# Performance work log

Measured on AMD Instinct MI355X. Metric: run time of the kernel, lower is better.

The kernel has to match this reference:

```python
import jax, jax.numpy as jnp
import numpy as np

MAX_N = 21
COORD = 3
TOTAL_T = 100
K_RANK = 3
POWER_STEPS = 10


def _recon_single(D, Wt, u_noise, x_noise):
    """D, Wt: [N,N]; u_noise: [K_RANK,N]; x_noise: [N,3]. Returns X: [N,3]."""
    N = MAX_N
    # dist_to_gram (classical MDS double-centering)
    D_row = jnp.sum(D, 0, keepdims=True) / N
    D_col = jnp.sum(D, 1, keepdims=True) / N
    D_mean = jnp.sum(D) / (N * N)
    B = -0.5 * (D - D_row - D_col + D_mean)
    # low_rank_approx_power: k=3 deflated power iterations, 10 steps each
    A = B
    us = []
    for i in range(K_RANK):
        u = u_noise[i]
        for _ in range(POWER_STEPS):
            # F.normalize(u, dim=0, p=2, eps=0.001)
            u = u / jnp.maximum(jnp.linalg.norm(u), 1e-3)
            u = A @ u
        eig_sq = jnp.sum(u * u)
        u = u / jnp.power(eig_sq + 0.01, 0.25)
        us.append(u)
        A = A - jnp.outer(u, u)
    X0 = jnp.stack(us, -1) + x_noise  # [N,3]

    T = jnp.float32(TOTAL_T)

    def energy(X):
        diff = X[None, :, :] - X[:, None, :]          # [N,N,3], D_X[i,j]=||X_j-X_i||^2
        D_X = jnp.sum(diff * diff, -1) + 0.01
        return jnp.sum(Wt * jnp.square(D - D_X))

    def step(X, t):
        g = jax.grad(energy)(X)
        dX = -0.1 * g
        speed = jnp.sqrt(jnp.sum(dX * dX, 1, keepdims=True) + 1e-3)
        alpha_t = 0.1 + (5.0 - 0.1) * ((T - t) / T)
        scale = alpha_t * jnp.tanh(speed / alpha_t) / speed
        return X + dX * scale, None

    X, _ = jax.lax.scan(step, X0, jnp.arange(TOTAL_T, dtype=jnp.float32))
    return X


def _forward(gnn_edge_out, W1, b1, W2, b2, u_noise, x_noise, batch_size):
    h_nf = W1.shape[1]
    # edge_mlp1 (MLP with 1 layer -> Linear + ReLU)
    edge_out = jax.nn.relu(gnn_edge_out @ W1 + b1)                     # [B*N*N, h]
    emb = jnp.sum(edge_out.reshape(batch_size, MAX_N, MAX_N, h_nf), axis=(1, 2))  # [B, h]
    # edge_mlp2 -> symmetrize -> softplus
    e2 = (edge_out @ W2 + b2).reshape(batch_size, MAX_N, MAX_N, 2)
    e2 = e2 + jnp.transpose(e2, (0, 2, 1, 3))
    dw = jax.nn.softplus(e2)
    D_init = dw[..., 0] * (1.0 - jnp.eye(MAX_N, dtype=dw.dtype))       # [B,N,N]
    W = dw[..., 1]                                                     # [B,N,N]
    X_pred = jax.vmap(_recon_single)(D_init, W, u_noise, x_noise)      # [B,N,3]
    return D_init, W, emb, X_pred


def setup_inputs() -> dict:
    key = jax.random.key(0)
    ks = jax.random.split(key, 5)
    B, h_nf = 1024, 256
    n_edges = B * MAX_N * MAX_N
    return {
        "gnn_edge_out": jax.random.normal(ks[0], (n_edges, h_nf), jnp.float32),
        "W1": jax.random.normal(ks[1], (h_nf, h_nf), jnp.float32) * (1.0 / np.sqrt(h_nf)),
        "b1": jnp.zeros((h_nf,), jnp.float32),
        "W2": jax.random.normal(ks[2], (h_nf, 2), jnp.float32) * (1.0 / np.sqrt(h_nf)),
        "b2": jnp.zeros((2,), jnp.float32),
        "u_noise": jax.random.normal(ks[3], (B, K_RANK, MAX_N), jnp.float32),
        "x_noise": jax.random.normal(ks[4], (B, MAX_N, COORD), jnp.float32),
        "batch_size": B,
    }


def reference(gnn_edge_out, W1, b1, W2, b2, u_noise, x_noise, batch_size):
    return _forward(gnn_edge_out, W1, b1, W2, b2, u_noise, x_noise, batch_size)
```

## Files before the change

### kernel.cpp

```cpp
#include <hip/hip_runtime.h>
#include <hip/hip_bf16.h>
#include <math.h>

#define B_SZ 1024
#define NMAX 21
#define NN 441
#define HNF 256
#define TOT_ROWS (B_SZ * NN)
#define TILES_PB 14
#define TROWS 32

typedef short short8 __attribute__((ext_vector_type(8)));
typedef float float4v __attribute__((ext_vector_type(4)));

__device__ __forceinline__ unsigned short f2bf(float x) {
    union { float f; unsigned int u; } v; v.f = x;
    unsigned int r = v.u + 0x7FFFu + ((v.u >> 16) & 1u);
    return (unsigned short)(r >> 16);
}

__device__ __forceinline__ unsigned pk_bf16(float lo, float hi) {
    __hip_bfloat162 h = __float22bfloat162_rn(float2{lo, hi});
    return *reinterpret_cast<unsigned*>(&h);
}

__device__ __forceinline__ float softplus_fast(float x) {
    float e = __builtin_amdgcn_exp2f(-fabsf(x) * 1.44269504088896f);
    float lg = __builtin_amdgcn_logf(1.f + e);
    return fmaxf(x, 0.f) + 0.69314718055995f * lg;
}

__device__ __forceinline__ float tanh_fast(float x) {
    float e = __builtin_amdgcn_exp2f(x * 2.8853900817779268f);
    float q = __builtin_amdgcn_rcpf(e + 1.f);
    return fmaf(-2.f, q, 1.f);
}

__global__ __launch_bounds__(256) void pack_w1(const float* __restrict__ W1,
                                               short* __restrict__ B0p,
                                               float* __restrict__ emb)
{
    int id = blockIdx.x * 256 + threadIdx.x;
    int j = id & 7, l = (id >> 3) & 63, f = (id >> 9) & 15, s = id >> 13;
    int k = s * 32 + ((l >> 4) << 3) + j;
    int c = (f << 4) + (l & 15);
    B0p[id] = (short)f2bf(W1[k * HNF + c]);
    #pragma unroll
    for (int e = 0; e < 4; e++)
        emb[(size_t)e * 65536 + id] = 0.f;
}

__global__ __launch_bounds__(256, 5) void fused_mlp_bf16(
    const float* __restrict__ gnn, const short* __restrict__ B0p,
    const float* __restrict__ b1, const float* __restrict__ W2,
    const float* __restrict__ b2,
    float* __restrict__ Dreg, float* __restrict__ Wreg, float* __restrict__ emb)
{
    __shared__ __align__(16) char ldsbuf[32768];
    float* stage = (float*)ldsbuf;
    short* Abf   = (short*)ldsbuf;
    float (*red0)[32] = (float(*)[32])(ldsbuf + 16384);
    float (*red1)[32] = (float(*)[32])(ldsbuf + 16384 + 512);

    const int t = threadIdx.x;
    const int w = t >> 6, l = t & 63;
    const int batch = blockIdx.x / TILES_PB;
    const int tile  = blockIdx.x % TILES_PB;
    const long row0 = (long)batch * NN + (long)tile * TROWS;
    const int vr = (tile == TILES_PB - 1) ? (NN - (TILES_PB - 1) * TROWS) : TROWS;

    #pragma unroll
    for (int i = 0; i < 8; i++) {
        int r = (w << 3) + i;
        long ar = row0 + r;
        if (ar >= (long)TOT_ROWS) ar = TOT_ROWS - 1;
        const float* gsrc = gnn + ar * HNF + (l << 2);
        __builtin_amdgcn_global_load_lds(
            (const __attribute__((address_space(1))) unsigned*)gsrc,
            (__attribute__((address_space(3))) unsigned*)(stage + (r << 8)),
            16, 0, 0);
    }

    uint2 pv[8];
    asm volatile("s_waitcnt vmcnt(4)" ::: "memory");
    #pragma unroll
    for (int i = 0; i < 4; i++) {
        float4 f = *(const float4*)(stage + (((w << 3) + i) << 8) + (l << 2));
        pv[i].x = pk_bf16(f.x, f.y);
        pv[i].y = pk_bf16(f.z, f.w);
    }
    asm volatile("s_waitcnt vmcnt(0)" ::: "memory");
    #pragma unroll
    for (int i = 4; i < 8; i++) {
        float4 f = *(const float4*)(stage + (((w << 3) + i) << 8) + (l << 2));
        pv[i].x = pk_bf16(f.x, f.y);
        pv[i].y = pk_bf16(f.z, f.w);
    }
    __syncthreads();

    const int kk_s = l >> 3;
    const int fk_s = (l >> 1) & 3;
    const int jh_s = l & 1;
    #pragma unroll
    for (int i = 0; i < 8; i++) {
        int r = (w << 3) + i;
        int di = (((kk_s << 1) + (r >> 4)) << 6) | (fk_s << 4) | (r & 15);
        *(uint2*)((char*)Abf + (((size_t)(di ^ kk_s)) << 4) + (jh_s << 3)) = pv[i];
    }
    __syncthreads();

    const int frow = l & 15;
    const int fk   = l >> 4;

    float4v acc[2][4];
    #pragma unroll
    for (int m = 0; m < 2; m++)
        #pragma unroll
        for (int n = 0; n < 4; n++)
            acc[m][n] = (float4v){0.f, 0.f, 0.f, 0.f};

    #pragma unroll 2
    for (int kk = 0; kk < 8; ++kk) {
        short8 bf[4], af[2];
        #pragma unroll
        for (int n = 0; n < 4; n++) {
            int nf = (w << 2) + n;
            size_t off = (size_t)((((kk << 4) + nf) << 6) | l) << 3;
            bf[n] = *(const short8*)(B0p + off);
        }
        #pragma unroll
        for (int m = 0; m < 2; m++) {
            int di = ((((kk << 1) + m) << 6) | l) ^ kk;
            af[m] = *(const short8*)(Abf + (size_t)di * 8);
        }
        #pragma unroll
        for (int m = 0; m < 2; m++)
            #pragma unroll
            for (int n = 0; n < 4; n++)
                acc[m][n] = __builtin_amdgcn_mfma_f32_16x16x32_bf16(af[m], bf[n], acc[m][n], 0, 0, 0);
    }

    float w20[4], w21[4], b1v[4];
    #pragma unroll
    for (int n = 0; n < 4; n++) {
        int cc = (((w << 2) + n) << 4) + frow;
        b1v[n] = b1[cc];
        w20[n] = W2[2 * cc];
        w21[n] = W2[2 * cc + 1];
    }
    float ps0[2][4], ps1[2][4], embp[4] = {0.f, 0.f, 0.f, 0.f};
    #pragma unroll
    for (int m = 0; m < 2; m++)
        #pragma unroll
        for (int j = 0; j < 4; j++) { ps0[m][j] = 0.f; ps1[m][j] = 0.f; }

    #pragma unroll
    for (int m = 0; m < 2; m++)
        #pragma unroll
        for (int n = 0; n < 4; n++)
            #pragma unroll
            for (int j = 0; j < 4; j++) {
                float h = fmaxf(acc[m][n][j] + b1v[n], 0.f);
                ps0[m][j] += h * w20[n];
                ps1[m][j] += h * w21[n];
                int row = (m << 4) + (fk << 2) + j;
                if (row < vr) embp[n] += h;
            }

    #pragma unroll
    for (int off = 1; off < 16; off <<= 1)
        #pragma unroll
        for (int m = 0; m < 2; m++)
            #pragma unroll
            for (int j = 0; j < 4; j++) {
                ps0[m][j] += __shfl_xor(ps0[m][j], off);
                ps1[m][j] += __shfl_xor(ps1[m][j], off);
            }
    if (frow == 0) {
        #pragma unroll
        for (int m = 0; m < 2; m++)
            #pragma unroll
            for (int j = 0; j < 4; j++) {
                int row = (m << 4) + (fk << 2) + j;
                red0[w][row] = ps0[m][j];
                red1[w][row] = ps1[m][j];
            }
    }

    #pragma unroll
    for (int n = 0; n < 4; n++) {
        embp[n] += __shfl_xor(embp[n], 16);
        embp[n] += __shfl_xor(embp[n], 32);
    }
    if (l < 16) {
        #pragma unroll
        for (int n = 0; n < 4; n++)
            atomicAdd(emb + (size_t)batch * 256 + (((w << 2) + n) << 4) + l, embp[n]);
    }

    __syncthreads();
    if (t < vr) {
        float v0 = b2[0] + red0[0][t] + red0[1][t] + red0[2][t] + red0[3][t];
        float v1 = b2[1] + red1[0][t] + red1[1][t] + red1[2][t] + red1[3][t];
        Dreg[row0 + t] = v0;
        Wreg[row0 + t] = v1;
    }
}

__global__ __launch_bounds__(64) void symrecon_kernel(
    float* __restrict__ Dreg, float* __restrict__ Wreg,
    const float* __restrict__ un, const float* __restrict__ xn,
    float* __restrict__ Xo)
{
    const int b = blockIdx.x, l = threadIdx.x;
    __shared__ float R0[NN], R1[NN];
    __shared__ float Rs[22], Us[22], Xs[3][22];

    float* Db = Dreg + (size_t)b * NN;
    float* Wb = Wreg + (size_t)b * NN;
    for (int idx = l; idx < NN; idx += 64) { R0[idx] = Db[idx]; R1[idx] = Wb[idx]; }
    if (l == 0) { Rs[21] = 0.f; Us[21] = 0.f; Xs[0][21] = 0.f; Xs[1][21] = 0.f; Xs[2][21] = 0.f; }
    __syncthreads();

    const int half = l >> 5;
    const int li   = l & 31;
    const bool act = li < NMAX;
    const int li0  = act ? li : 0;
    const int q0   = half * 11;

    float Drow[11], Wrow[11], WD[11];
    float rsh = 0.f;
    #pragma unroll
    for (int j = 0; j < 11; j++) {
        int q = q0 + j;
        bool v = act && (q < NMAX);
        int qc = v ? q : 0;
        float rd = R0[li0 * NMAX + qc] + R0[qc * NMAX + li0];
        float rw = R1[li0 * NMAX + qc] + R1[qc * NMAX + li0];
        float d  = (v && q != li) ? softplus_fast(rd) : 0.f;
        float wv = v ? softplus_fast(rw) : 0.f;
        Drow[j] = d; Wrow[j] = wv; WD[j] = wv * d;
        rsh += d;
    }
    if (act) {
        #pragma unroll
        for (int j = 0; j < 11; j++) {
            int q = q0 + j;
            if (q < NMAX) {
                Db[li * NMAX + q] = Drow[j];
                Wb[li * NMAX + q] = Wrow[j];
            }
        }
    }

    float rsf = rsh + __shfl_xor(rsh, 32);
    float tot = rsh;
    #pragma unroll
    for (int m = 1; m < 64; m <<= 1) tot += __shfl_xor(tot, m);
    const float mean = tot * (1.f / (float)NN);
    const float rsn  = rsf * (1.f / (float)NMAX);
    if (act && half == 0) Rs[li] = rsn;
    float Arow[11];
    #pragma unroll
    for (int j = 0; j < 11; j++) {
        int q = q0 + j;
        bool v = act && (q < NMAX);
        float rsq = Rs[q];
        Arow[j] = v ? -0.5f * (Drow[j] - rsn - rsq + mean) : 0.f;
    }

    float xc[3];
    #pragma unroll
    for (int e = 0; e < 3; e++) {
        float u = act ? un[(size_t)b * 63 + e * NMAX + li] : 0.f;
        for (int s = 0; s < 10; s++) {
            float n2 = (act && half == 0) ? u * u : 0.f;
            #pragma unroll
            for (int m = 1; m < 64; m <<= 1) n2 += __shfl_xor(n2, m);
            u *= fminf(__builtin_amdgcn_rsqf(n2), 1000.f);
            if (act && half == 0) Us[li] = u;
            float a = 0.f;
            #pragma unroll
            for (int j = 0; j < 11; j++) a = fmaf(Arow[j], Us[q0 + j], a);
            a += __shfl_xor(a, 32);
            u = act ? a : 0.f;
        }
        float e2 = (act && half == 0) ? u * u : 0.f;
        #pragma unroll
        for (int m = 1; m < 64; m <<= 1) e2 += __shfl_xor(e2, m);
        u *= sqrtf(__builtin_amdgcn_rsqf(e2 + 0.01f));
        xc[e] = u;
        if (act && half == 0) Us[li] = u;
        #pragma unroll
        for (int j = 0; j < 11; j++) Arow[j] = fmaf(-u, Us[q0 + j], Arow[j]);
    }
    float x = xc[0], y = xc[1], z = xc[2];
    if (act) {
        x += xn[(size_t)b * 63 + li * 3 + 0];
        y += xn[(size_t)b * 63 + li * 3 + 1];
        z += xn[(size_t)b * 63 + li * 3 + 2];
    }
    if (act && half == 0) { Xs[0][li] = x; Xs[1][li] = y; Xs[2][li] = z; }

    for (int tstep = 0; tstep < 100; tstep++) {
        float gx = 0.f, gy = 0.f, gz = 0.f;
        #pragma unroll
        for (int j = 0; j < 11; j++) {
            int q = q0 + j;
            float dx = x - Xs[0][q];
            float dy = y - Xs[1][q];
            float dz = z - Xs[2][q];
            float s  = fmaf(dx, dx, fmaf(dy, dy, fmaf(dz, dz, 0.01f)));
            float cm = fmaf(-Wrow[j], s, WD[j]);
            gx = fmaf(cm, dx, gx);
            gy = fmaf(cm, dy, gy);
            gz = fmaf(cm, dz, gz);
        }
        gx += __shfl_xor(gx, 32);
        gy += __shfl_xor(gy, 32);
        gz += __shfl_xor(gz, 32);
        float d0 = 0.8f * gx, d1 = 0.8f * gy, d2 = 0.8f * gz;
        float ss = fmaf(d0, d0, fmaf(d1, d1, fmaf(d2, d2, 1e-3f)));
        float inv_sp = __builtin_amdgcn_rsqf(ss);
        float speed  = ss * inv_sp;
        float alpha  = fmaf(-0.049f, (float)tstep, 5.0f);
        float th     = tanh_fast(speed * __builtin_amdgcn_rcpf(alpha));
        float scale  = alpha * th * inv_sp;
        x = fmaf(d0, scale, x);
        y = fmaf(d1, scale, y);
        z = fmaf(d2, scale, z);
        if (act && half == 0) { Xs[0][li] = x; Xs[1][li] = y; Xs[2][li] = z; }
    }
    if (act && half == 0) {
        Xo[(size_t)b * 63 + li * 3 + 0] = x;
        Xo[(size_t)b * 63 + li * 3 + 1] = y;
        Xo[(size_t)b * 63 + li * 3 + 2] = z;
    }
}

extern "C" void kernel_launch(void* const* d_in, const int* in_sizes, int n_in,
                              void* d_out, int out_size, void* d_ws, size_t ws_size,
                              hipStream_t stream) {
    const float* gnn = (const float*)d_in[0];
    const float* W1  = (const float*)d_in[1];
    const float* b1  = (const float*)d_in[2];
    const float* W2  = (const float*)d_in[3];
    const float* b2  = (const float*)d_in[4];
    const float* un  = (const float*)d_in[5];
    const float* xn  = (const float*)d_in[6];

    float* out  = (float*)d_out;
    float* Dreg = out;
    float* Wreg = out + (size_t)TOT_ROWS;
    float* emb  = out + (size_t)2 * TOT_ROWS;
    float* Xo   = out + (size_t)2 * TOT_ROWS + B_SZ*256;

    short* B0p = (short*)d_ws;

    pack_w1<<<dim3(256), dim3(256), 0, stream>>>(W1, B0p, emb);

    fused_mlp_bf16<<<dim3(B_SZ * TILES_PB), dim3(256), 0, stream>>>(
        gnn, B0p, b1, W2, b2, Dreg, Wreg, emb);

    symrecon_kernel<<<dim3(B_SZ), dim3(64), 0, stream>>>(Dreg, Wreg, un, xn, Xo);
}
```

Measured before the change: 243.5 us.

## Process two row tiles per block, prefetching second tile into registers during first GEMM

Each workgroup of the fused MLP kernel now handles two adjacent 32-row tiles. The second tile is prefetched with plain global loads into registers while the first tile goes through LDS staging, MFMA and the epilogue. This hides load latency and halves the number of emb atomics per batch. In exchange it raises register pressure (launch bounds drop from 5 to 4 waves) and halves the grid size.

```diff
diff --git a/kernel.cpp b/kernel.cpp
--- a/kernel.cpp
+++ b/kernel.cpp
@@ -50,7 +50,7 @@
         emb[(size_t)e * 65536 + id] = 0.f;
 }
 
-__global__ __launch_bounds__(256, 5) void fused_mlp_bf16(
+__global__ __launch_bounds__(256, 4) void fused_mlp_bf16(
     const float* __restrict__ gnn, const short* __restrict__ B0p,
     const float* __restrict__ b1, const float* __restrict__ W2,
     const float* __restrict__ b2,
@@ -64,81 +64,38 @@
 
     const int t = threadIdx.x;
     const int w = t >> 6, l = t & 63;
-    const int batch = blockIdx.x / TILES_PB;
-    const int tile  = blockIdx.x % TILES_PB;
-    const long row0 = (long)batch * NN + (long)tile * TROWS;
-    const int vr = (tile == TILES_PB - 1) ? (NN - (TILES_PB - 1) * TROWS) : TROWS;
+    const int batch = blockIdx.x / 7;
+    const int pair  = blockIdx.x % 7;
+    const int tileA = pair * 2;
+    const int tileB = pair * 2 + 1;
+    const long rowA = (long)batch * NN + (long)tileA * TROWS;
+    const long rowB = (long)batch * NN + (long)tileB * TROWS;
+    const int vrB = (tileB == TILES_PB - 1) ? (NN - (TILES_PB - 1) * TROWS) : TROWS;
+
+    const int kk_s = l >> 3;
+    const int fk_s = (l >> 1) & 3;
+    const int jh_s = l & 1;
+    const int frow = l & 15;
+    const int fk   = l >> 4;
 
     #pragma unroll
     for (int i = 0; i < 8; i++) {
         int r = (w << 3) + i;
-        long ar = row0 + r;
-        if (ar >= (long)TOT_ROWS) ar = TOT_ROWS - 1;
+        long ar = rowA + r;
         const float* gsrc = gnn + ar * HNF + (l << 2);
         __builtin_amdgcn_global_load_lds(
             (const __attribute__((address_space(1))) unsigned*)gsrc,
             (__attribute__((address_space(3))) unsigned*)(stage + (r << 8)),
             16, 0, 0);
     }
-
-    uint2 pv[8];
-    asm volatile("s_waitcnt vmcnt(4)" ::: "memory");
-    #pragma unroll
-    for (int i = 0; i < 4; i++) {
-        float4 f = *(const float4*)(stage + (((w << 3) + i) << 8) + (l << 2));
-        pv[i].x = pk_bf16(f.x, f.y);
-        pv[i].y = pk_bf16(f.z, f.w);
-    }
-    asm volatile("s_waitcnt vmcnt(0)" ::: "memory");
-    #pragma unroll
-    for (int i = 4; i < 8; i++) {
-        float4 f = *(const float4*)(stage + (((w << 3) + i) << 8) + (l << 2));
-        pv[i].x = pk_bf16(f.x, f.y);
-        pv[i].y = pk_bf16(f.z, f.w);
-    }
-    __syncthreads();
-
-    const int kk_s = l >> 3;
-    const int fk_s = (l >> 1) & 3;
-    const int jh_s = l & 1;
+    float4 fb[8];
     #pragma unroll
     for (int i = 0; i < 8; i++) {
-        int r = (w << 3) + i;
-        int di = (((kk_s << 1) + (r >> 4)) << 6) | (fk_s << 4) | (r & 15);
-        *(uint2*)((char*)Abf + (((size_t)(di ^ kk_s)) << 4) + (jh_s << 3)) = pv[i];
-    }
-    __syncthreads();
-
-    const int frow = l & 15;
-    const int fk   = l >> 4;
-
-    float4v acc[2][4];
-    #pragma unroll
-    for (int m = 0; m < 2; m++)
-        #pragma unroll
-        for (int n = 0; n < 4; n++)
-            acc[m][n] = (float4v){0.f, 0.f, 0.f, 0.f};
-
-    #pragma unroll 2
-    for (int kk = 0; kk < 8; ++kk) {
-        short8 bf[4], af[2];
-        #pragma unroll
-        for (int n = 0; n < 4; n++) {
-            int nf = (w << 2) + n;
-            size_t off = (size_t)((((kk << 4) + nf) << 6) | l) << 3;
-            bf[n] = *(const short8*)(B0p + off);
-        }
-        #pragma unroll
-        for (int m = 0; m < 2; m++) {
-            int di = ((((kk << 1) + m) << 6) | l) ^ kk;
-            af[m] = *(const short8*)(Abf + (size_t)di * 8);
-        }
-        #pragma unroll
-        for (int m = 0; m < 2; m++)
-            #pragma unroll
-            for (int n = 0; n < 4; n++)
-                acc[m][n] = __builtin_amdgcn_mfma_f32_16x16x32_bf16(af[m], bf[n], acc[m][n], 0, 0, 0);
-    }
+        long ar = rowB + (w << 3) + i;
+        if (ar >= (long)TOT_ROWS) ar = TOT_ROWS - 1;
+        fb[i] = *(const float4*)(gnn + ar * HNF + (l << 2));
+    }
+    asm volatile("" ::: "memory");
 
     float w20[4], w21[4], b1v[4];
     #pragma unroll
@@ -148,43 +105,191 @@
         w20[n] = W2[2 * cc];
         w21[n] = W2[2 * cc + 1];
     }
-    float ps0[2][4], ps1[2][4], embp[4] = {0.f, 0.f, 0.f, 0.f};
+
+    uint2 pv[8];
+    asm volatile("s_waitcnt vmcnt(12)" ::: "memory");
+    #pragma unroll
+    for (int i = 0; i < 4; i++) {
+        float4 f = *(const float4*)(stage + (((w << 3) + i) << 8) + (l << 2));
+        pv[i].x = pk_bf16(f.x, f.y);
+        pv[i].y = pk_bf16(f.z, f.w);
+    }
+    asm volatile("s_waitcnt vmcnt(8)" ::: "memory");
+    #pragma unroll
+    for (int i = 4; i < 8; i++) {
+        float4 f = *(const float4*)(stage + (((w << 3) + i) << 8) + (l << 2));
+        pv[i].x = pk_bf16(f.x, f.y);
+        pv[i].y = pk_bf16(f.z, f.w);
+    }
+    __syncthreads();
+    #pragma unroll
+    for (int i = 0; i < 8; i++) {
+        int r = (w << 3) + i;
+        int di = (((kk_s << 1) + (r >> 4)) << 6) | (fk_s << 4) | (r & 15);
+        *(uint2*)((char*)Abf + (((size_t)(di ^ kk_s)) << 4) + (jh_s << 3)) = pv[i];
+    }
+    __syncthreads();
+
+    float4v acc[2][4];
     #pragma unroll
     for (int m = 0; m < 2; m++)
         #pragma unroll
-        for (int j = 0; j < 4; j++) { ps0[m][j] = 0.f; ps1[m][j] = 0.f; }
+        for (int n = 0; n < 4; n++)
+            acc[m][n] = (float4v){0.f, 0.f, 0.f, 0.f};
+
+    #pragma unroll 2
+    for (int kk = 0; kk < 8; ++kk) {
+        short8 bf[4], af[2];
+        #pragma unroll
+        for (int n = 0; n < 4; n++) {
+            int nf = (w << 2) + n;
+            size_t off = (size_t)((((kk << 4) + nf) << 6) | l) << 3;
+            bf[n] = *(const short8*)(B0p + off);
+        }
+        #pragma unroll
+        for (int m = 0; m < 2; m++) {
+            int di = ((((kk << 1) + m) << 6) | l) ^ kk;
+            af[m] = *(const short8*)(Abf + (size_t)di * 8);
+        }
+        #pragma unroll
+        for (int m = 0; m < 2; m++)
+            #pragma unroll
+            for (int n = 0; n < 4; n++)
+                acc[m][n] = __builtin_amdgcn_mfma_f32_16x16x32_bf16(af[m], bf[n], acc[m][n], 0, 0, 0);
+    }
+
+    float embp[4] = {0.f, 0.f, 0.f, 0.f};
+    {
+        float ps0[2][4], ps1[2][4];
+        #pragma unroll
+        for (int m = 0; m < 2; m++)
+            #pragma unroll
+            for (int j = 0; j < 4; j++) { ps0[m][j] = 0.f; ps1[m][j] = 0.f; }
+        #pragma unroll
+        for (int m = 0; m < 2; m++)
+            #pragma unroll
+            for (int n = 0; n < 4; n++)
+                #pragma unroll
+                for (int j = 0; j < 4; j++) {
+                    float h = fmaxf(acc[m][n][j] + b1v[n], 0.f);
+                    ps0[m][j] += h * w20[n];
+                    ps1[m][j] += h * w21[n];
+                    embp[n] += h;
+                }
+        #pragma unroll
+        for (int off = 1; off < 16; off <<= 1)
+            #pragma unroll
+            for (int m = 0; m < 2; m++)
+                #pragma unroll
+                for (int j = 0; j < 4; j++) {
+                    ps0[m][j] += __shfl_xor(ps0[m][j], off);
+                    ps1[m][j] += __shfl_xor(ps1[m][j], off);
+                }
+        if (frow == 0) {
+            #pragma unroll
+            for (int m = 0; m < 2; m++)
+                #pragma unroll
+                for (int j = 0; j < 4; j++) {
+                    int row = (m << 4) + (fk << 2) + j;
+                    red0[w][row] = ps0[m][j];
+                    red1[w][row] = ps1[m][j];
+                }
+        }
+        __syncthreads();
+        if (t < TROWS) {
+            float v0 = b2[0] + red0[0][t] + red0[1][t] + red0[2][t] + red0[3][t];
+            float v1 = b2[1] + red1[0][t] + red1[1][t] + red1[2][t] + red1[3][t];
+            Dreg[rowA + t] = v0;
+            Wreg[rowA + t] = v1;
+        }
+    }
+
+    asm volatile("s_waitcnt vmcnt(0)" ::: "memory");
+    #pragma unroll
+    for (int i = 0; i < 8; i++) {
+        pv[i].x = pk_bf16(fb[i].x, fb[i].y);
+        pv[i].y = pk_bf16(fb[i].z, fb[i].w);
+    }
+    #pragma unroll
+    for (int i = 0; i < 8; i++) {
+        int r = (w << 3) + i;
+        int di = (((kk_s << 1) + (r >> 4)) << 6) | (fk_s << 4) | (r & 15);
+        *(uint2*)((char*)Abf + (((size_t)(di ^ kk_s)) << 4) + (jh_s << 3)) = pv[i];
+    }
+    __syncthreads();
 
     #pragma unroll
     for (int m = 0; m < 2; m++)
         #pragma unroll
         for (int n = 0; n < 4; n++)
-            #pragma unroll
-            for (int j = 0; j < 4; j++) {
-                float h = fmaxf(acc[m][n][j] + b1v[n], 0.f);
-                ps0[m][j] += h * w20[n];
-                ps1[m][j] += h * w21[n];
-                int row = (m << 4) + (fk << 2) + j;
-                if (row < vr) embp[n] += h;
-            }
-
-    #pragma unroll
-    for (int off = 1; off < 16; off <<= 1)
-        #pragma unroll
-        for (int m = 0; m < 2; m++)
-            #pragma unroll
-            for (int j = 0; j < 4; j++) {
-                ps0[m][j] += __shfl_xor(ps0[m][j], off);
-                ps1[m][j] += __shfl_xor(ps1[m][j], off);
-            }
-    if (frow == 0) {
-        #pragma unroll
-        for (int m = 0; m < 2; m++)
-            #pragma unroll
-            for (int j = 0; j < 4; j++) {
-                int row = (m << 4) + (fk << 2) + j;
-                red0[w][row] = ps0[m][j];
-                red1[w][row] = ps1[m][j];
-            }
+            acc[m][n] = (float4v){0.f, 0.f, 0.f, 0.f};
+
+    #pragma unroll 2
+    for (int kk = 0; kk < 8; ++kk) {
+        short8 bf[4], af[2];
+        #pragma unroll
+        for (int n = 0; n < 4; n++) {
+            int nf = (w << 2) + n;
+            size_t off = (size_t)((((kk << 4) + nf) << 6) | l) << 3;
+            bf[n] = *(const short8*)(B0p + off);
+        }
+        #pragma unroll
+        for (int m = 0; m < 2; m++) {
+            int di = ((((kk << 1) + m) << 6) | l) ^ kk;
+            af[m] = *(const short8*)(Abf + (size_t)di * 8);
+        }
+        #pragma unroll
+        for (int m = 0; m < 2; m++)
+            #pragma unroll
+            for (int n = 0; n < 4; n++)
+                acc[m][n] = __builtin_amdgcn_mfma_f32_16x16x32_bf16(af[m], bf[n], acc[m][n], 0, 0, 0);
+    }
+
+    {
+        float ps0[2][4], ps1[2][4];
+        #pragma unroll
+        for (int m = 0; m < 2; m++)
+            #pragma unroll
+            for (int j = 0; j < 4; j++) { ps0[m][j] = 0.f; ps1[m][j] = 0.f; }
+        #pragma unroll
+        for (int m = 0; m < 2; m++)
+            #pragma unroll
+            for (int n = 0; n < 4; n++)
+                #pragma unroll
+                for (int j = 0; j < 4; j++) {
+                    float h = fmaxf(acc[m][n][j] + b1v[n], 0.f);
+                    ps0[m][j] += h * w20[n];
+                    ps1[m][j] += h * w21[n];
+                    int row = (m << 4) + (fk << 2) + j;
+                    if (row < vrB) embp[n] += h;
+                }
+        #pragma unroll
+        for (int off = 1; off < 16; off <<= 1)
+            #pragma unroll
+            for (int m = 0; m < 2; m++)
+                #pragma unroll
+                for (int j = 0; j < 4; j++) {
+                    ps0[m][j] += __shfl_xor(ps0[m][j], off);
+                    ps1[m][j] += __shfl_xor(ps1[m][j], off);
+                }
+        __syncthreads();
+        if (frow == 0) {
+            #pragma unroll
+            for (int m = 0; m < 2; m++)
+                #pragma unroll
+                for (int j = 0; j < 4; j++) {
+                    int row = (m << 4) + (fk << 2) + j;
+                    red0[w][row] = ps0[m][j];
+                    red1[w][row] = ps1[m][j];
+                }
+        }
+        __syncthreads();
+        if (t < vrB) {
+            float v0 = b2[0] + red0[0][t] + red0[1][t] + red0[2][t] + red0[3][t];
+            float v1 = b2[1] + red1[0][t] + red1[1][t] + red1[2][t] + red1[3][t];
+            Dreg[rowB + t] = v0;
+            Wreg[rowB + t] = v1;
+        }
     }
 
     #pragma unroll
@@ -196,14 +301,6 @@
         #pragma unroll
         for (int n = 0; n < 4; n++)
             atomicAdd(emb + (size_t)batch * 256 + (((w << 2) + n) << 4) + l, embp[n]);
-    }
-
-    __syncthreads();
-    if (t < vr) {
-        float v0 = b2[0] + red0[0][t] + red0[1][t] + red0[2][t] + red0[3][t];
-        float v1 = b2[1] + red1[0][t] + red1[1][t] + red1[2][t] + red1[3][t];
-        Dreg[row0 + t] = v0;
-        Wreg[row0 + t] = v1;
     }
 }
 
@@ -359,7 +456,7 @@
 
     pack_w1<<<dim3(256), dim3(256), 0, stream>>>(W1, B0p, emb);
 
-    fused_mlp_bf16<<<dim3(B_SZ * TILES_PB), dim3(256), 0, stream>>>(
+    fused_mlp_bf16<<<dim3(B_SZ * 7), dim3(256), 0, stream>>>(
         gnn, B0p, b1, W2, b2, Dreg, Wreg, emb);
 
     symrecon_kernel<<<dim3(B_SZ), dim3(64), 0, stream>>>(Dreg, Wreg, un, xn, Xo);
```

Result: slower. 251.9 us (+3.4%).
